# Performance work log

Hardware: AMD Instinct MI355X
Metric: run time of the kernel (lower is better)

Reference implementation:

```python
import math
import jax, jax.numpy as jnp
import numpy as np

K = 16
EPS = 1e-05
EPS_VAR = 1e-04


def _gelu(x):
    # tanh-approx GELU, identical to the torch module's _gelu
    c = math.sqrt(2.0 / math.pi)
    return 0.5 * x * (1.0 + jnp.tanh(c * (x + 0.044715 * x ** 3)))


def setup_inputs() -> dict:
    key = jax.random.key(0)
    k1, k2, k3, k4 = jax.random.split(key, 4)
    B, T, D = 4, 4096, 4096
    x = jax.random.normal(k1, (B, T, D), dtype=jnp.float32)
    ema_mean = 0.1 * jax.random.normal(k2, (D,), dtype=jnp.float32)
    # ensure variance is positive and realistic
    ema_sq = ema_mean ** 2 + jax.random.uniform(k3, (D,), dtype=jnp.float32, minval=0.5, maxval=1.5)
    ema_out = jax.random.normal(k4, (D,), dtype=jnp.float32)
    return {
        "x": x,
        "ema_mean": ema_mean,
        "ema_sq": ema_sq,
        "ema_out": ema_out,
        "log_tau": jnp.asarray(math.log(2.0), dtype=jnp.float32),
        "log_beta_up": jnp.asarray(math.log(math.exp(0.5) - 1.0), dtype=jnp.float32),
        "log_gamma": jnp.asarray(math.log(math.exp(1.0) - 1.0), dtype=jnp.float32),
        "logit_beta_fam": jnp.asarray(-1.386, dtype=jnp.float32),
    }


def reference(x, ema_mean, ema_sq, ema_out, log_tau, log_beta_up, log_gamma, logit_beta_fam):
    sg = jax.lax.stop_gradient
    B, T, D = x.shape
    k = min(K, D // 2)

    # scalar params (tau is only used inside torch.no_grad -> stop-grad)
    tau = sg(jnp.exp(log_tau))
    beta_up = jax.nn.softplus(log_beta_up)
    gamma = jax.nn.softplus(log_gamma)
    beta_fam = jax.nn.sigmoid(logit_beta_fam)

    out = _gelu(x)  # [B,T,D], differentiable path

    # ----- no_grad z-score + top/bot-k index selection -----
    mu = sg(ema_mean)
    var = jnp.maximum(sg(ema_sq) - mu ** 2, EPS_VAR)
    std = jnp.sqrt(var)
    z = (sg(x) - mu) / (std + EPS)          # [B,T,D], detached
    abs_z = jnp.abs(z)
    _, topk_idx = jax.lax.top_k(abs_z, k)   # [B,T,k] largest |z|
    _, botk_idx = jax.lax.top_k(-abs_z, k)  # [B,T,k] smallest |z|

    # ----- gate construction (gather + scatter along D) -----
    z_topk = jnp.take_along_axis(z, topk_idx, axis=-1)            # [B,T,k]
    g_topk = jnp.clip(1.0 + beta_up * jnp.tanh(gamma * z_topk), 0.1, 8.0)

    N = B * T
    rows = jnp.arange(N)[:, None]                                  # [N,1]
    gate = jnp.ones((N, D), dtype=x.dtype)
    gate = gate.at[rows, topk_idx.reshape(N, k)].set(g_topk.reshape(N, k))
    gate = gate.at[rows, botk_idx.reshape(N, k)].set(
        jnp.broadcast_to(beta_fam.astype(x.dtype), (N, k)))
    gate = gate.reshape(B, T, D)

    # ----- cosine-similarity gate (all no_grad) -----
    out_d = sg(out)
    out_n = out_d / jnp.maximum(jnp.linalg.norm(out_d, axis=-1, keepdims=True), 1e-12)
    eo = sg(ema_out)
    ema_n = eo / jnp.maximum(jnp.linalg.norm(eo), 1e-12)           # [D]
    cos_sim = jnp.clip(jnp.sum(out_n * ema_n, axis=-1), -1.0, 1.0)  # [B,T]
    gate_cos = jnp.exp(-tau * cos_sim)[..., None]                   # [B,T,1]

    return out * gate * gate_cos
```

## Files before the change

kernel.cpp:

```cpp
#include <hip/hip_runtime.h>
#include <stdint.h>

#define TPB   256
#define D_DIM 4096
#define WPB   4
#define ITERS 16
#define CAP   128
#define KSEL  16
#define THI0  2.5f
#define TLO0  0.02f

#define WS_STDP 0
#define WS_MI   D_DIM
#define WS_SCAL (2*D_DIM)
#define WS_GC   8200
#define WS_REC_F 24584

typedef float vfloat4 __attribute__((ext_vector_type(4)));

__device__ __forceinline__ float fast_rcp(float v)  { return __builtin_amdgcn_rcpf(v); }
__device__ __forceinline__ float fast_exp2(float v) { return __builtin_amdgcn_exp2f(v); }

#define GELU_AN (-2.30220819f)
#define GELU_BN (-0.10294331f)
#define TWO_LOG2E (2.8853900817779268f)
#define LOG2E     (1.4426950408889634f)

__device__ __forceinline__ float gelu_fast(float x) {
    float x2 = x * x;
    float s  = fmaf(x2, GELU_BN, GELU_AN);
    float nq = x * s;
    float ex = fast_exp2(nq);
    return x * fast_rcp(1.0f + ex);
}

__device__ __forceinline__ float tanh_fast_pm(float y2l) {
    float ex = fast_exp2(y2l);
    float r  = fast_rcp(1.0f + ex);
    return fmaf(-2.0f, r, 1.0f);
}

__device__ __forceinline__ float top_gate(float zz, float beta_up, float kg) {
    float g = fmaf(beta_up, tanh_fast_pm(zz * kg), 1.0f);
    return fminf(fmaxf(g, 0.1f), 8.0f);
}

__device__ __forceinline__ unsigned long long make_key_top(float zp, unsigned int d) {
    const unsigned int zb = __float_as_uint(zp);
    const unsigned int pb = zb & 0x7fffffffu;
    const unsigned int klo = 0xFFFFE000u | ((~d & 0xFFFu) << 1) | (zb >> 31);
    return ((unsigned long long)pb << 32) | klo;
}
__device__ __forceinline__ unsigned long long make_key_bot(float zp, unsigned int d) {
    const unsigned int zb = __float_as_uint(zp);
    const unsigned int pb = (zb & 0x7fffffffu) ^ 0x7fffffffu;
    const unsigned int klo = 0xFFFFE000u | ((~d & 0xFFFu) << 1) | (zb >> 31);
    return ((unsigned long long)pb << 32) | klo;
}

__device__ __forceinline__ unsigned int bf16_hi(float v) {
    unsigned int u = __float_as_uint(v);
    u = (u + 0x7FFFu + ((u >> 16) & 1u)) >> 16;
    return u & 0xFFFFu;
}

__global__ __launch_bounds__(256) void precomp(
    const float* __restrict__ em, const float* __restrict__ eq,
    const float* __restrict__ eo,
    const float* __restrict__ lt, const float* __restrict__ lb,
    const float* __restrict__ lg, const float* __restrict__ lf,
    float* __restrict__ ws)
{
    __shared__ float red[4];
    const int tid = threadIdx.x;
    unsigned int* wsu = (unsigned int*)ws;
    float e2 = 0.0f;
    for (int i = 0; i < D_DIM / 256; ++i) {
        const int d = i * 256 + tid;
        const float mu  = em[d];
        const float mu2 = __fmul_rn(mu, mu);
        float var = __fsub_rn(eq[d], mu2);
        var = fmaxf(var, 1e-4f);
        const float stdp = __fadd_rn(sqrtf(var), 1e-5f);
        ws[WS_STDP + d] = stdp;
        const float invv = 1.0f / stdp;
        wsu[WS_MI + d] = (bf16_hi(mu) << 16) | bf16_hi(invv);
        const float e = eo[d];
        e2 = fmaf(e, e, e2);
    }
    #pragma unroll
    for (int off = 32; off; off >>= 1) e2 += __shfl_xor(e2, off);
    if ((tid & 63) == 0) red[tid >> 6] = e2;
    __syncthreads();
    if (tid == 0) {
        const float t  = red[0] + red[1] + red[2] + red[3];
        const float en = sqrtf(t);
        ws[WS_SCAL + 0] = expf(lt[0]);
        ws[WS_SCAL + 1] = log1pf(expf(lb[0]));
        ws[WS_SCAL + 2] = log1pf(expf(lg[0]));
        ws[WS_SCAL + 3] = 1.0f / (1.0f + expf(-lf[0]));
        ws[WS_SCAL + 4] = 1.0f / fmaxf(en, 1e-12f);
    }
}

__global__ __launch_bounds__(TPB) void fused_gelu_gate(
    const float* __restrict__ x,
    const float* __restrict__ ema_mean,
    const float* __restrict__ ema_out,
    float* __restrict__ ws,
    unsigned long long* __restrict__ recs,
    float* __restrict__ out)
{
    __shared__ unsigned long long lists[WPB][2 * CAP];
    __shared__ unsigned int cnt[WPB][2];
    const int tid = threadIdx.x;
    const int ln  = tid & 63;
    const int wv  = tid >> 6;
    const int row = blockIdx.x * WPB + wv;
    const long long base = (long long)row * D_DIM;

    if (ln < 2) cnt[wv][ln] = 0u;

    const float tau      = ws[WS_SCAL + 0];
    const float beta_up  = ws[WS_SCAL + 1];
    const float kg       = ws[WS_SCAL + 2] * TWO_LOG2E;
    const float beta_fam = ws[WS_SCAL + 3];
    const float inv_en   = ws[WS_SCAL + 4];
    const unsigned int* mip = (const unsigned int*)ws + WS_MI;

    float s_o2 = 0.0f, s_dot = 0.0f;
    unsigned long long maskT = 0ull, maskB = 0ull;

    #pragma unroll
    for (int i = 0; i < ITERS; ++i) {
        const int off = (i * 64 + ln) * 4;
        const float4 xv = *(const float4*)(x + base + off);
        const uint4  mv = *(const uint4*)(mip + off);
        const float4 ev = *(const float4*)(ema_out + off);
        const float xs[4] = {xv.x, xv.y, xv.z, xv.w};
        const unsigned int mis[4] = {mv.x, mv.y, mv.z, mv.w};
        const float es[4] = {ev.x, ev.y, ev.z, ev.w};
        #pragma unroll
        for (int j = 0; j < 4; ++j) {
            const int e = i * 4 + j;
            const float xx = xs[j];
            const float mu = __uint_as_float(mis[j] & 0xFFFF0000u);
            const float iv = __uint_as_float(mis[j] << 16);
            const float zz = (xx - mu) * iv;
            const float og = gelu_fast(xx);
            s_o2  = fmaf(og, og, s_o2);
            s_dot = fmaf(og, es[j], s_dot);
            const float az = fabsf(zz);
            maskT |= (az >= THI0) ? (1ull << e) : 0ull;
            maskB |= (az <= TLO0) ? (1ull << e) : 0ull;
        }
    }

    #pragma unroll
    for (int off = 32; off; off >>= 1) {
        s_o2  += __shfl_xor(s_o2, off);
        s_dot += __shfl_xor(s_dot, off);
    }
    const float on = sqrtf(s_o2);
    float cs = (s_dot * inv_en) / fmaxf(on, 1e-12f);
    cs = fminf(fmaxf(cs, -1.0f), 1.0f);
    const float gc = fast_exp2(-tau * cs * LOG2E);
    if (ln == 0) ws[WS_GC + row] = gc;

    #pragma unroll
    for (int i = 0; i < ITERS; ++i) {
        const int off = (i * 64 + ln) * 4;
        const float4 xv = *(const float4*)(x + base + off);
        vfloat4 ov;
        ov.x = gelu_fast(xv.x) * gc;
        ov.y = gelu_fast(xv.y) * gc;
        ov.z = gelu_fast(xv.z) * gc;
        ov.w = gelu_fast(xv.w) * gc;
        __builtin_nontemporal_store(ov, (vfloat4*)(out + base + off));
    }

    {
        unsigned long long mT = maskT;
        while (mT) {
            const int b = __ffsll(mT) - 1; mT &= mT - 1ull;
            const unsigned int d = (unsigned int)(((b >> 2) * 64 + ln) * 4 + (b & 3));
            const float xx   = x[base + d];
            const float mu   = ema_mean[d];
            const float stdp = ws[WS_STDP + d];
            const float zp   = __fdiv_rn(__fsub_rn(xx, mu), stdp);
            const unsigned int p = atomicAdd(&cnt[wv][0], 1u);
            if (p < CAP) lists[wv][p] = make_key_top(zp, d);
        }
        unsigned long long mB = maskB;
        while (mB) {
            const int b = __ffsll(mB) - 1; mB &= mB - 1ull;
            const unsigned int d = (unsigned int)(((b >> 2) * 64 + ln) * 4 + (b & 3));
            const float xx   = x[base + d];
            const float mu   = ema_mean[d];
            const float stdp = ws[WS_STDP + d];
            const float zp   = __fdiv_rn(__fsub_rn(xx, mu), stdp);
            const unsigned int p = atomicAdd(&cnt[wv][1], 1u);
            if (p < CAP) lists[wv][CAP + p] = make_key_bot(zp, d);
        }
    }
    __threadfence_block();

    {
        unsigned int cT = cnt[wv][0], cB = cnt[wv][1];
        float thi = THI0, tlo = TLO0;
        int tries = 0;
        while ((cT < (unsigned)KSEL || cT > (unsigned)CAP ||
                cB < (unsigned)KSEL || cB > (unsigned)CAP) && tries < 20) {
            if (cT < (unsigned)KSEL) thi *= 0.5f; else if (cT > (unsigned)CAP) thi *= 1.5f;
            if (cB < (unsigned)KSEL) tlo *= 2.0f; else if (cB > (unsigned)CAP) tlo *= 0.6666f;
            if (ln < 2) cnt[wv][ln] = 0u;
            __threadfence_block();
            for (int e = 0; e < 64; ++e) {
                const unsigned int d = (unsigned int)(((e >> 2) * 64 + ln) * 4 + (e & 3));
                const float xx   = x[base + d];
                const float mu   = ema_mean[d];
                const float stdp = ws[WS_STDP + d];
                const float zp   = __fdiv_rn(__fsub_rn(xx, mu), stdp);
                const float az   = fabsf(zp);
                if (az >= thi) {
                    const unsigned int p = atomicAdd(&cnt[wv][0], 1u);
                    if (p < CAP) lists[wv][p] = make_key_top(zp, d);
                } else if (az <= tlo) {
                    const unsigned int p = atomicAdd(&cnt[wv][1], 1u);
                    if (p < CAP) lists[wv][CAP + p] = make_key_bot(zp, d);
                }
            }
            __threadfence_block();
            cT = cnt[wv][0]; cB = cnt[wv][1];
            ++tries;
        }
    }

    #pragma unroll
    for (int half = 0; half < 2; ++half) {
        const unsigned int m = min(cnt[wv][half], (unsigned)CAP);
        const unsigned long long* lp = &lists[wv][half * CAP];
        const unsigned long long k0 = (ln < (int)m) ? lp[ln] : 0ull;
        const unsigned long long k1 = (ln + 64 < (int)m) ? lp[ln + 64] : 0ull;
        unsigned int r0 = 0, r1 = 0;
        for (unsigned int j = 0; j < m; ++j) {
            const unsigned long long kj = lp[j];
            r0 += (kj > k0) ? 1u : 0u;
            r1 += (kj > k1) ? 1u : 0u;
        }
        #pragma unroll
        for (int s = 0; s < 2; ++s) {
            const unsigned long long k_i = s ? k1 : k0;
            const unsigned int rank = s ? r1 : r0;
            const bool valid = s ? (ln + 64 < (int)m) : (ln < (int)m);
            if (valid && rank < (unsigned)KSEL) {
                const unsigned int klo = (unsigned int)(k_i & 0xffffffffu);
                const unsigned int d   = (~(klo >> 1)) & 0xFFFu;
                float g;
                if (half == 0) {
                    const unsigned int pb = (unsigned int)(k_i >> 32);
                    const float azf = __uint_as_float(pb);
                    const float zw  = (klo & 1u) ? -azf : azf;
                    g = top_gate(zw, beta_up, kg);
                } else {
                    g = beta_fam;
                }
                recs[(long long)row * 32 + half * KSEL + rank] =
                    ((unsigned long long)__float_as_uint(g) << 32) | d;
            }
        }
    }
}

__global__ __launch_bounds__(256) void fixup(
    const float* __restrict__ x,
    const float* __restrict__ ws,
    const unsigned long long* __restrict__ recs,
    float* __restrict__ out)
{
    const int gid = blockIdx.x * 256 + threadIdx.x;
    const unsigned long long rec = recs[gid];
    const unsigned int d = (unsigned int)(rec & 0xFFFFu);
    if (d < (unsigned)D_DIM) {
        const int row = gid >> 5;
        const float gc = ws[WS_GC + row];
        const float g  = __uint_as_float((unsigned int)(rec >> 32));
        const long long idx = (long long)row * D_DIM + d;
        out[idx] = gelu_fast(x[idx]) * g * gc;
    }
}

extern "C" void kernel_launch(void* const* d_in, const int* in_sizes, int n_in,
                              void* d_out, int out_size, void* d_ws, size_t ws_size,
                              hipStream_t stream) {
    const float* x  = (const float*)d_in[0];
    const float* em = (const float*)d_in[1];
    const float* eq = (const float*)d_in[2];
    const float* eo = (const float*)d_in[3];
    const float* lt = (const float*)d_in[4];
    const float* lb = (const float*)d_in[5];
    const float* lg = (const float*)d_in[6];
    const float* lf = (const float*)d_in[7];
    float* o  = (float*)d_out;
    float* ws = (float*)d_ws;
    unsigned long long* recs = (unsigned long long*)(ws + WS_REC_F);
    const int rows = in_sizes[0] / D_DIM;
    precomp<<<dim3(1), dim3(256), 0, stream>>>(em, eq, eo, lt, lb, lg, lf, ws);
    fused_gelu_gate<<<dim3(rows / WPB), dim3(TPB), 0, stream>>>(x, em, eo, ws, recs, o);
    fixup<<<dim3(rows * 32 / 256), dim3(256), 0, stream>>>(x, ws, recs, o);
}
```

Baseline: 209.5 us.

## Stage per-column stats in LDS, loop rows per wave, precompute fixup values

The main kernel now loads ema_mean, the std, and ema_out into shared memory once per block. It uses 512-thread blocks where each wave walks 4 rows, instead of re-reading the packed bf16 mu/inv-std table from global memory for every row. Candidate selection no longer uses bitmasks and a second pass. It compares |x-mu| against threshold*std inline and computes the exact z and list insertion immediately, avoiding a division per element. The fixup kernel now just writes final values computed in the main kernel, so it no longer re-reads x or gc. The costs are 48KB of LDS per block plus larger blocks, which may reduce occupancy, and divergent atomics inside the hot loop. Fewer blocks also means less parallelism across the GPU.

```diff
diff --git a/kernel.cpp b/kernel.cpp
--- a/kernel.cpp
+++ b/kernel.cpp
@@ -1,9 +1,10 @@
 #include <hip/hip_runtime.h>
 #include <stdint.h>
 
-#define TPB   256
+#define TPB   512
+#define WPB   (TPB/64)
+#define RPW   4
 #define D_DIM 4096
-#define WPB   4
 #define ITERS 16
 #define CAP   128
 #define KSEL  16
@@ -11,7 +12,6 @@
 #define TLO0  0.02f
 
 #define WS_STDP 0
-#define WS_MI   D_DIM
 #define WS_SCAL (2*D_DIM)
 #define WS_GC   8200
 #define WS_REC_F 24584
@@ -56,12 +56,6 @@
     const unsigned int pb = (zb & 0x7fffffffu) ^ 0x7fffffffu;
     const unsigned int klo = 0xFFFFE000u | ((~d & 0xFFFu) << 1) | (zb >> 31);
     return ((unsigned long long)pb << 32) | klo;
-}
-
-__device__ __forceinline__ unsigned int bf16_hi(float v) {
-    unsigned int u = __float_as_uint(v);
-    u = (u + 0x7FFFu + ((u >> 16) & 1u)) >> 16;
-    return u & 0xFFFFu;
 }
 
 __global__ __launch_bounds__(256) void precomp(
@@ -73,7 +67,6 @@
 {
     __shared__ float red[4];
     const int tid = threadIdx.x;
-    unsigned int* wsu = (unsigned int*)ws;
     float e2 = 0.0f;
     for (int i = 0; i < D_DIM / 256; ++i) {
         const int d = i * 256 + tid;
@@ -83,8 +76,6 @@
         var = fmaxf(var, 1e-4f);
         const float stdp = __fadd_rn(sqrtf(var), 1e-5f);
         ws[WS_STDP + d] = stdp;
-        const float invv = 1.0f / stdp;
-        wsu[WS_MI + d] = (bf16_hi(mu) << 16) | bf16_hi(invv);
         const float e = eo[d];
         e2 = fmaf(e, e, e2);
     }
@@ -111,170 +102,170 @@
     unsigned long long* __restrict__ recs,
     float* __restrict__ out)
 {
+    __shared__ float muS[D_DIM];
+    __shared__ float sdS[D_DIM];
+    __shared__ float evS[D_DIM];
     __shared__ unsigned long long lists[WPB][2 * CAP];
     __shared__ unsigned int cnt[WPB][2];
     const int tid = threadIdx.x;
     const int ln  = tid & 63;
     const int wv  = tid >> 6;
-    const int row = blockIdx.x * WPB + wv;
-    const long long base = (long long)row * D_DIM;
-
-    if (ln < 2) cnt[wv][ln] = 0u;
+
+    #pragma unroll
+    for (int k = 0; k < D_DIM / (TPB * 4); ++k) {
+        const int off = (k * TPB + tid) * 4;
+        *(float4*)&muS[off] = *(const float4*)(ema_mean + off);
+        *(float4*)&sdS[off] = *(const float4*)(ws + WS_STDP + off);
+        *(float4*)&evS[off] = *(const float4*)(ema_out + off);
+    }
+    __syncthreads();
 
     const float tau      = ws[WS_SCAL + 0];
     const float beta_up  = ws[WS_SCAL + 1];
     const float kg       = ws[WS_SCAL + 2] * TWO_LOG2E;
     const float beta_fam = ws[WS_SCAL + 3];
     const float inv_en   = ws[WS_SCAL + 4];
-    const unsigned int* mip = (const unsigned int*)ws + WS_MI;
-
-    float s_o2 = 0.0f, s_dot = 0.0f;
-    unsigned long long maskT = 0ull, maskB = 0ull;
-
-    #pragma unroll
-    for (int i = 0; i < ITERS; ++i) {
-        const int off = (i * 64 + ln) * 4;
-        const float4 xv = *(const float4*)(x + base + off);
-        const uint4  mv = *(const uint4*)(mip + off);
-        const float4 ev = *(const float4*)(ema_out + off);
-        const float xs[4] = {xv.x, xv.y, xv.z, xv.w};
-        const unsigned int mis[4] = {mv.x, mv.y, mv.z, mv.w};
-        const float es[4] = {ev.x, ev.y, ev.z, ev.w};
+
+    for (int r = 0; r < RPW; ++r) {
+        const int row = blockIdx.x * (WPB * RPW) + wv * RPW + r;
+        const long long base = (long long)row * D_DIM;
+
+        if (ln < 2) cnt[wv][ln] = 0u;
+        __threadfence_block();
+
+        float s_o2 = 0.0f, s_dot = 0.0f;
+
         #pragma unroll
-        for (int j = 0; j < 4; ++j) {
-            const int e = i * 4 + j;
-            const float xx = xs[j];
-            const float mu = __uint_as_float(mis[j] & 0xFFFF0000u);
-            const float iv = __uint_as_float(mis[j] << 16);
-            const float zz = (xx - mu) * iv;
-            const float og = gelu_fast(xx);
-            s_o2  = fmaf(og, og, s_o2);
-            s_dot = fmaf(og, es[j], s_dot);
-            const float az = fabsf(zz);
-            maskT |= (az >= THI0) ? (1ull << e) : 0ull;
-            maskB |= (az <= TLO0) ? (1ull << e) : 0ull;
-        }
-    }
-
-    #pragma unroll
-    for (int off = 32; off; off >>= 1) {
-        s_o2  += __shfl_xor(s_o2, off);
-        s_dot += __shfl_xor(s_dot, off);
-    }
-    const float on = sqrtf(s_o2);
-    float cs = (s_dot * inv_en) / fmaxf(on, 1e-12f);
-    cs = fminf(fmaxf(cs, -1.0f), 1.0f);
-    const float gc = fast_exp2(-tau * cs * LOG2E);
-    if (ln == 0) ws[WS_GC + row] = gc;
-
-    #pragma unroll
-    for (int i = 0; i < ITERS; ++i) {
-        const int off = (i * 64 + ln) * 4;
-        const float4 xv = *(const float4*)(x + base + off);
-        vfloat4 ov;
-        ov.x = gelu_fast(xv.x) * gc;
-        ov.y = gelu_fast(xv.y) * gc;
-        ov.z = gelu_fast(xv.z) * gc;
-        ov.w = gelu_fast(xv.w) * gc;
-        __builtin_nontemporal_store(ov, (vfloat4*)(out + base + off));
-    }
-
-    {
-        unsigned long long mT = maskT;
-        while (mT) {
-            const int b = __ffsll(mT) - 1; mT &= mT - 1ull;
-            const unsigned int d = (unsigned int)(((b >> 2) * 64 + ln) * 4 + (b & 3));
-            const float xx   = x[base + d];
-            const float mu   = ema_mean[d];
-            const float stdp = ws[WS_STDP + d];
-            const float zp   = __fdiv_rn(__fsub_rn(xx, mu), stdp);
-            const unsigned int p = atomicAdd(&cnt[wv][0], 1u);
-            if (p < CAP) lists[wv][p] = make_key_top(zp, d);
-        }
-        unsigned long long mB = maskB;
-        while (mB) {
-            const int b = __ffsll(mB) - 1; mB &= mB - 1ull;
-            const unsigned int d = (unsigned int)(((b >> 2) * 64 + ln) * 4 + (b & 3));
-            const float xx   = x[base + d];
-            const float mu   = ema_mean[d];
-            const float stdp = ws[WS_STDP + d];
-            const float zp   = __fdiv_rn(__fsub_rn(xx, mu), stdp);
-            const unsigned int p = atomicAdd(&cnt[wv][1], 1u);
-            if (p < CAP) lists[wv][CAP + p] = make_key_bot(zp, d);
-        }
-    }
-    __threadfence_block();
-
-    {
-        unsigned int cT = cnt[wv][0], cB = cnt[wv][1];
-        float thi = THI0, tlo = TLO0;
-        int tries = 0;
-        while ((cT < (unsigned)KSEL || cT > (unsigned)CAP ||
-                cB < (unsigned)KSEL || cB > (unsigned)CAP) && tries < 20) {
-            if (cT < (unsigned)KSEL) thi *= 0.5f; else if (cT > (unsigned)CAP) thi *= 1.5f;
-            if (cB < (unsigned)KSEL) tlo *= 2.0f; else if (cB > (unsigned)CAP) tlo *= 0.6666f;
-            if (ln < 2) cnt[wv][ln] = 0u;
-            __threadfence_block();
-            for (int e = 0; e < 64; ++e) {
-                const unsigned int d = (unsigned int)(((e >> 2) * 64 + ln) * 4 + (e & 3));
-                const float xx   = x[base + d];
-                const float mu   = ema_mean[d];
-                const float stdp = ws[WS_STDP + d];
-                const float zp   = __fdiv_rn(__fsub_rn(xx, mu), stdp);
-                const float az   = fabsf(zp);
-                if (az >= thi) {
+        for (int i = 0; i < ITERS; ++i) {
+            const int off = (i * 64 + ln) * 4;
+            const float4 xv = *(const float4*)(x + base + off);
+            const float4 mv = *(const float4*)&muS[off];
+            const float4 sv = *(const float4*)&sdS[off];
+            const float4 ev = *(const float4*)&evS[off];
+            const float xs[4] = {xv.x, xv.y, xv.z, xv.w};
+            const float ms[4] = {mv.x, mv.y, mv.z, mv.w};
+            const float ss[4] = {sv.x, sv.y, sv.z, sv.w};
+            const float es[4] = {ev.x, ev.y, ev.z, ev.w};
+            #pragma unroll
+            for (int j = 0; j < 4; ++j) {
+                const float xx = xs[j];
+                const float sd = ss[j];
+                const float diff = __fsub_rn(xx, ms[j]);
+                const float ad = fabsf(diff);
+                const float og = gelu_fast(xx);
+                s_o2  = fmaf(og, og, s_o2);
+                s_dot = fmaf(og, es[j], s_dot);
+                if (ad >= THI0 * sd) {
+                    const unsigned int d = (unsigned int)(off + j);
+                    const float zp = __fdiv_rn(diff, sd);
                     const unsigned int p = atomicAdd(&cnt[wv][0], 1u);
                     if (p < CAP) lists[wv][p] = make_key_top(zp, d);
-                } else if (az <= tlo) {
+                } else if (ad <= TLO0 * sd) {
+                    const unsigned int d = (unsigned int)(off + j);
+                    const float zp = __fdiv_rn(diff, sd);
                     const unsigned int p = atomicAdd(&cnt[wv][1], 1u);
                     if (p < CAP) lists[wv][CAP + p] = make_key_bot(zp, d);
                 }
             }
-            __threadfence_block();
-            cT = cnt[wv][0]; cB = cnt[wv][1];
-            ++tries;
-        }
-    }
-
-    #pragma unroll
-    for (int half = 0; half < 2; ++half) {
-        const unsigned int m = min(cnt[wv][half], (unsigned)CAP);
-        const unsigned long long* lp = &lists[wv][half * CAP];
-        const unsigned long long k0 = (ln < (int)m) ? lp[ln] : 0ull;
-        const unsigned long long k1 = (ln + 64 < (int)m) ? lp[ln + 64] : 0ull;
-        unsigned int r0 = 0, r1 = 0;
-        for (unsigned int j = 0; j < m; ++j) {
-            const unsigned long long kj = lp[j];
-            r0 += (kj > k0) ? 1u : 0u;
-            r1 += (kj > k1) ? 1u : 0u;
-        }
+        }
+
         #pragma unroll
-        for (int s = 0; s < 2; ++s) {
-            const unsigned long long k_i = s ? k1 : k0;
-            const unsigned int rank = s ? r1 : r0;
-            const bool valid = s ? (ln + 64 < (int)m) : (ln < (int)m);
-            if (valid && rank < (unsigned)KSEL) {
-                const unsigned int klo = (unsigned int)(k_i & 0xffffffffu);
-                const unsigned int d   = (~(klo >> 1)) & 0xFFFu;
-                float g;
-                if (half == 0) {
-                    const unsigned int pb = (unsigned int)(k_i >> 32);
-                    const float azf = __uint_as_float(pb);
-                    const float zw  = (klo & 1u) ? -azf : azf;
-                    g = top_gate(zw, beta_up, kg);
-                } else {
-                    g = beta_fam;
+        for (int off = 32; off; off >>= 1) {
+            s_o2  += __shfl_xor(s_o2, off);
+            s_dot += __shfl_xor(s_dot, off);
+        }
+        const float on = sqrtf(s_o2);
+        float cs = (s_dot * inv_en) / fmaxf(on, 1e-12f);
+        cs = fminf(fmaxf(cs, -1.0f), 1.0f);
+        const float gc = fast_exp2(-tau * cs * LOG2E);
+        if (ln == 0) ws[WS_GC + row] = gc;
+
+        #pragma unroll
+        for (int i = 0; i < ITERS; ++i) {
+            const int off = (i * 64 + ln) * 4;
+            const float4 xv = *(const float4*)(x + base + off);
+            vfloat4 ov;
+            ov.x = gelu_fast(xv.x) * gc;
+            ov.y = gelu_fast(xv.y) * gc;
+            ov.z = gelu_fast(xv.z) * gc;
+            ov.w = gelu_fast(xv.w) * gc;
+            __builtin_nontemporal_store(ov, (vfloat4*)(out + base + off));
+        }
+        __threadfence_block();
+
+        {
+            unsigned int cT = cnt[wv][0], cB = cnt[wv][1];
+            float thi = THI0, tlo = TLO0;
+            int tries = 0;
+            while ((cT < (unsigned)KSEL || cT > (unsigned)CAP ||
+                    cB < (unsigned)KSEL || cB > (unsigned)CAP) && tries < 20) {
+                if (cT < (unsigned)KSEL) thi *= 0.5f; else if (cT > (unsigned)CAP) thi *= 1.5f;
+                if (cB < (unsigned)KSEL) tlo *= 2.0f; else if (cB > (unsigned)CAP) tlo *= 0.6666f;
+                if (ln < 2) cnt[wv][ln] = 0u;
+                __threadfence_block();
+                for (int e = 0; e < 64; ++e) {
+                    const unsigned int d = (unsigned int)(((e >> 2) * 64 + ln) * 4 + (e & 3));
+                    const float xx   = x[base + d];
+                    const float mu   = muS[d];
+                    const float sd   = sdS[d];
+                    const float diff = __fsub_rn(xx, mu);
+                    const float ad   = fabsf(diff);
+                    if (ad >= thi * sd) {
+                        const float zp = __fdiv_rn(diff, sd);
+                        const unsigned int p = atomicAdd(&cnt[wv][0], 1u);
+                        if (p < CAP) lists[wv][p] = make_key_top(zp, d);
+                    } else if (ad <= tlo * sd) {
+                        const float zp = __fdiv_rn(diff, sd);
+                        const unsigned int p = atomicAdd(&cnt[wv][1], 1u);
+                        if (p < CAP) lists[wv][CAP + p] = make_key_bot(zp, d);
+                    }
                 }
-                recs[(long long)row * 32 + half * KSEL + rank] =
-                    ((unsigned long long)__float_as_uint(g) << 32) | d;
+                __threadfence_block();
+                cT = cnt[wv][0]; cB = cnt[wv][1];
+                ++tries;
             }
         }
+
+        #pragma unroll
+        for (int half = 0; half < 2; ++half) {
+            const unsigned int m = min(cnt[wv][half], (unsigned)CAP);
+            const unsigned long long* lp = &lists[wv][half * CAP];
+            const unsigned long long k0 = (ln < (int)m) ? lp[ln] : 0ull;
+            const unsigned long long k1 = (ln + 64 < (int)m) ? lp[ln + 64] : 0ull;
+            unsigned int r0 = 0, r1 = 0;
+            for (unsigned int j = 0; j < m; ++j) {
+                const unsigned long long kj = lp[j];
+                r0 += (kj > k0) ? 1u : 0u;
+                r1 += (kj > k1) ? 1u : 0u;
+            }
+            #pragma unroll
+            for (int s = 0; s < 2; ++s) {
+                const unsigned long long k_i = s ? k1 : k0;
+                const unsigned int rank = s ? r1 : r0;
+                const bool valid = s ? (ln + 64 < (int)m) : (ln < (int)m);
+                if (valid && rank < (unsigned)KSEL) {
+                    const unsigned int klo = (unsigned int)(k_i & 0xffffffffu);
+                    const unsigned int d   = (~(klo >> 1)) & 0xFFFu;
+                    float g;
+                    if (half == 0) {
+                        const unsigned int pb = (unsigned int)(k_i >> 32);
+                        const float azf = __uint_as_float(pb);
+                        const float zw  = (klo & 1u) ? -azf : azf;
+                        g = top_gate(zw, beta_up, kg);
+                    } else {
+                        g = beta_fam;
+                    }
+                    const float xx = x[base + d];
+                    const float val = gelu_fast(xx) * g * gc;
+                    recs[(long long)row * 32 + half * KSEL + rank] =
+                        ((unsigned long long)__float_as_uint(val) << 32) | d;
+                }
+            }
+        }
     }
 }
 
 __global__ __launch_bounds__(256) void fixup(
-    const float* __restrict__ x,
-    const float* __restrict__ ws,
     const unsigned long long* __restrict__ recs,
     float* __restrict__ out)
 {
@@ -283,10 +274,8 @@
     const unsigned int d = (unsigned int)(rec & 0xFFFFu);
     if (d < (unsigned)D_DIM) {
         const int row = gid >> 5;
-        const float gc = ws[WS_GC + row];
-        const float g  = __uint_as_float((unsigned int)(rec >> 32));
         const long long idx = (long long)row * D_DIM + d;
-        out[idx] = gelu_fast(x[idx]) * g * gc;
+        out[idx] = __uint_as_float((unsigned int)(rec >> 32));
     }
 }
 
@@ -306,6 +295,6 @@
     unsigned long long* recs = (unsigned long long*)(ws + WS_REC_F);
     const int rows = in_sizes[0] / D_DIM;
     precomp<<<dim3(1), dim3(256), 0, stream>>>(em, eq, eo, lt, lb, lg, lf, ws);
-    fused_gelu_gate<<<dim3(rows / WPB), dim3(TPB), 0, stream>>>(x, em, eo, ws, recs, o);
-    fixup<<<dim3(rows * 32 / 256), dim3(256), 0, stream>>>(x, ws, recs, o);
-}
+    fused_gelu_gate<<<dim3(rows / (WPB * RPW)), dim3(TPB), 0, stream>>>(x, em, eo, ws, recs, o);
+    fixup<<<dim3(rows * 32 / 256), dim3(256), 0, stream>>>(recs, o);
+}
```

Result: slower. 337.0 us (+60.8%).
